# Kernel optimization log

Hardware: AMD Instinct MI355X
Metric: run time of the kernel (lower is better)

## Reference

```python
import jax, jax.numpy as jnp
import numpy as np

WD = 11
HF = WD // 2  # 5

def _offsets():
    # Reproduce the torch module's expanding-ring offset ordering exactly.
    offs = []
    for i in range(1, HF + 1):
        for v in range(HF - i, HF + i + 1):
            for u in range(HF - i, HF + i + 1):
                if not (u == HF and v == HF) and (u, v) not in offs:
                    offs.append((u, v))
    return offs  # length WD*WD-1 = 120

_OFFS = _offsets()


def setup_inputs() -> dict:
    key = jax.random.key(0)
    x = jax.random.normal(key, (2, 3, 384, 1280), dtype=jnp.float32)
    return {"x": x, "attack": 1}


def reference(x, attack):
    n, c, h, w = x.shape
    xm = jnp.mean(x, axis=1)  # [n,h,w] grayscale
    xp = jnp.pad(xm, ((0, 0), (HF, HF), (HF, HF)), mode="reflect")  # [n,h+2*HF,w+2*HF]
    # All 120 shifted views in ring order; static slices, stacked on channel dim.
    shifted = jnp.stack([xp[:, v:v + h, u:u + w] for (u, v) in _OFFS], axis=1)  # [n,120,h,w]
    center = xm[:, None, :, :]
    if attack:
        return jax.nn.sigmoid((shifted - center) * 100000.0)
    return shifted >= center
```

## Files before the change

kernel.cpp:

```cpp
#include <hip/hip_runtime.h>
#include <cstddef>
#include <cstdint>

constexpr int N_  = 2;
constexpr int C_  = 3;
constexpr int H_  = 384;
constexpr int W_  = 1280;
constexpr int HWp = H_ * W_;
constexpr int NOFF = 120;
constexpr int HF_  = 5;

__host__ __device__ constexpr int k_of(int u, int v) {
    int du = u - HF_, dv = v - HF_;
    int au = du < 0 ? -du : du;
    int av = dv < 0 ? -dv : dv;
    int r = au > av ? au : av;
    if (r == 0) return -1;
    int base = (2 * r - 1) * (2 * r - 1) - 1;
    int dv2 = v - (HF_ - r);
    int du2 = u - (HF_ - r);
    int idx = 0;
    if (dv2 == 0)            idx = du2;
    else if (dv2 == 2 * r)   idx = (2 * r + 1) + 2 * (2 * r - 1) + du2;
    else                     idx = (2 * r + 1) + 2 * (dv2 - 1) + (du2 == 0 ? 0 : 1);
    return base + idx;
}

__global__ __launch_bounds__(256) void mean_kernel(const float* __restrict__ x,
                                                   float* __restrict__ xm) {
    int i = blockIdx.x * 256 + threadIdx.x;
    constexpr int TOT4 = N_ * HWp / 4;
    if (i >= TOT4) return;
    int n = i / (HWp / 4);
    int j = i - n * (HWp / 4);
    const float4* x0 = (const float4*)(x + (size_t)n * C_ * HWp);
    const float4* x1 = (const float4*)(x + (size_t)n * C_ * HWp + HWp);
    const float4* x2 = (const float4*)(x + (size_t)n * C_ * HWp + 2 * HWp);
    float4 a = x0[j], b = x1[j], c = x2[j];
    float4 m;
    m.x = (a.x + b.x + c.x) / 3.0f;
    m.y = (a.y + b.y + c.y) / 3.0f;
    m.z = (a.z + b.z + c.z) / 3.0f;
    m.w = (a.w + b.w + c.w) / 3.0f;
    ((float4*)xm)[i] = m;
}

__device__ __forceinline__ float census_val(float s, float center) {
    float d = s - center;
    float r;
    if (__builtin_expect(fabsf(d) >= 1.6e-4f, 1)) {
        r = d > 0.0f ? 1.0f : 0.0f;
    } else {
        float e = __expf(d * -100000.0f);
        r = __builtin_amdgcn_rcpf(1.0f + e);
    }
    return r;
}

__global__ __launch_bounds__(256) void census4_kernel(const float* __restrict__ xm,
                                                      float* __restrict__ out) {
    constexpr int TOT = N_ * HWp / 4;
    int g = blockIdx.x * 256 + threadIdx.x;
    if (g >= TOT) return;
    int n   = g / (HWp / 4);
    int rem = g - n * (HWp / 4);
    int y   = rem / (W_ / 4);
    int x0  = (rem - y * (W_ / 4)) * 4;

    const float* xmn = xm + (size_t)n * HWp;
    float4 c4 = *(const float4*)(xmn + (size_t)y * W_ + x0);

    int xr[14];
#pragma unroll
    for (int j = 0; j < 14; ++j) {
        int xx = x0 - HF_ + j;
        xx = xx < 0 ? -xx : xx;
        xx = xx >= W_ ? 2 * (W_ - 1) - xx : xx;
        xr[j] = xx;
    }

    float* outp = out + (size_t)n * NOFF * HWp + (size_t)y * W_ + x0;

#pragma unroll
    for (int v = 0; v < 11; ++v) {
        int yy = y + v - HF_;
        yy = yy < 0 ? -yy : yy;
        yy = yy >= H_ ? 2 * (H_ - 1) - yy : yy;
        const float* row = xmn + (size_t)yy * W_;

        float s[14];
#pragma unroll
        for (int j = 0; j < 14; ++j) s[j] = row[xr[j]];

#pragma unroll
        for (int u = 0; u < 11; ++u) {
            if (u == HF_ && v == HF_) continue;
            const int k = k_of(u, v);
            float4 r;
            r.x = census_val(s[u + 0], c4.x);
            r.y = census_val(s[u + 1], c4.y);
            r.z = census_val(s[u + 2], c4.z);
            r.w = census_val(s[u + 3], c4.w);
            *(float4*)(outp + (size_t)k * HWp) = r;
        }
    }
}

__device__ __forceinline__ float mean3(const float* __restrict__ xn, int off) {
    return (xn[off] + xn[off + HWp] + xn[off + 2 * HWp]) / 3.0f;
}

__global__ __launch_bounds__(256) void census_fused_kernel(const float* __restrict__ x,
                                                           float* __restrict__ out) {
    int bx = blockIdx.x % 5;
    int t  = blockIdx.x / 5;
    int y  = t % H_;
    int n  = t / H_;
    int xp = bx * 256 + threadIdx.x;

    const float* xn = x + (size_t)n * C_ * HWp;
    float center = mean3(xn, y * W_ + xp);

    int xr[11];
#pragma unroll
    for (int u = 0; u < 11; ++u) {
        int xx = xp + u - HF_;
        xx = xx < 0 ? -xx : xx;
        xx = xx >= W_ ? 2 * (W_ - 1) - xx : xx;
        xr[u] = xx;
    }

    float* outp = out + (size_t)n * NOFF * HWp + (size_t)y * W_ + xp;

#pragma unroll
    for (int v = 0; v < 11; ++v) {
        int yy = y + v - HF_;
        yy = yy < 0 ? -yy : yy;
        yy = yy >= H_ ? 2 * (H_ - 1) - yy : yy;
#pragma unroll
        for (int u = 0; u < 11; ++u) {
            if (u == HF_ && v == HF_) continue;
            const int k = k_of(u, v);
            float s = mean3(xn, yy * W_ + xr[u]);
            outp[(size_t)k * HWp] = census_val(s, center);
        }
    }
}

extern "C" void kernel_launch(void* const* d_in, const int* in_sizes, int n_in,
                              void* d_out, int out_size, void* d_ws, size_t ws_size,
                              hipStream_t stream) {
    const float* x = (const float*)d_in[0];
    float* out = (float*)d_out;

    const size_t xm_bytes = (size_t)N_ * HWp * sizeof(float);

    if (ws_size >= xm_bytes) {
        float* xm = (float*)d_ws;
        const int mean_blocks = (N_ * HWp / 4 + 255) / 256;
        mean_kernel<<<mean_blocks, 256, 0, stream>>>(x, xm);
        const int census_blocks = (N_ * HWp / 4 + 255) / 256;
        census4_kernel<<<census_blocks, 256, 0, stream>>>(xm, out);
    } else {
        const int census_blocks = N_ * H_ * (W_ / 256);
        census_fused_kernel<<<census_blocks, 256, 0, stream>>>(x, out);
    }
}
```

Baseline: 470.8 us.

## Fuse channel mean into census kernel via LDS halo tiles with nontemporal stores

Replaces the separate mean kernel and global-memory census kernel with one kernel. Each block computes the grayscale mean for a 4x256 tile plus its reflect-padded halo into shared memory, then reads neighbours from LDS. Output writes use nontemporal stores so the large output streams past the cache. This removes the intermediate workspace round trip and a kernel launch, at the cost of recomputing halo means, since the 14x266 tile redundantly covers a 4-row output tile.

```diff
diff --git a/kernel.cpp b/kernel.cpp
--- a/kernel.cpp
+++ b/kernel.cpp
@@ -9,6 +9,11 @@
 constexpr int HWp = H_ * W_;
 constexpr int NOFF = 120;
 constexpr int HF_  = 5;
+
+constexpr int TW = 256;
+constexpr int TH = 4;
+constexpr int SW = TW + 2 * HF_;
+constexpr int SH = TH + 2 * HF_;
 
 __host__ __device__ constexpr int k_of(int u, int v) {
     int du = u - HF_, dv = v - HF_;
@@ -26,25 +31,6 @@
     return base + idx;
 }
 
-__global__ __launch_bounds__(256) void mean_kernel(const float* __restrict__ x,
-                                                   float* __restrict__ xm) {
-    int i = blockIdx.x * 256 + threadIdx.x;
-    constexpr int TOT4 = N_ * HWp / 4;
-    if (i >= TOT4) return;
-    int n = i / (HWp / 4);
-    int j = i - n * (HWp / 4);
-    const float4* x0 = (const float4*)(x + (size_t)n * C_ * HWp);
-    const float4* x1 = (const float4*)(x + (size_t)n * C_ * HWp + HWp);
-    const float4* x2 = (const float4*)(x + (size_t)n * C_ * HWp + 2 * HWp);
-    float4 a = x0[j], b = x1[j], c = x2[j];
-    float4 m;
-    m.x = (a.x + b.x + c.x) / 3.0f;
-    m.y = (a.y + b.y + c.y) / 3.0f;
-    m.z = (a.z + b.z + c.z) / 3.0f;
-    m.w = (a.w + b.w + c.w) / 3.0f;
-    ((float4*)xm)[i] = m;
-}
-
 __device__ __forceinline__ float census_val(float s, float center) {
     float d = s - center;
     float r;
@@ -57,92 +43,64 @@
     return r;
 }
 
-__global__ __launch_bounds__(256) void census4_kernel(const float* __restrict__ xm,
-                                                      float* __restrict__ out) {
-    constexpr int TOT = N_ * HWp / 4;
-    int g = blockIdx.x * 256 + threadIdx.x;
-    if (g >= TOT) return;
-    int n   = g / (HWp / 4);
-    int rem = g - n * (HWp / 4);
-    int y   = rem / (W_ / 4);
-    int x0  = (rem - y * (W_ / 4)) * 4;
+typedef float f32x4 __attribute__((ext_vector_type(4)));
 
-    const float* xmn = xm + (size_t)n * HWp;
-    float4 c4 = *(const float4*)(xmn + (size_t)y * W_ + x0);
+__global__ __launch_bounds__(256) void census_fused_lds(const float* __restrict__ x,
+                                                        float* __restrict__ out) {
+    __shared__ float sm[SH][SW];
 
-    int xr[14];
-#pragma unroll
-    for (int j = 0; j < 14; ++j) {
-        int xx = x0 - HF_ + j;
-        xx = xx < 0 ? -xx : xx;
-        xx = xx >= W_ ? 2 * (W_ - 1) - xx : xx;
-        xr[j] = xx;
+    int bx = blockIdx.x % (W_ / TW);
+    int t  = blockIdx.x / (W_ / TW);
+    int yt = t % (H_ / TH);
+    int n  = t / (H_ / TH);
+    int x0 = bx * TW, y0 = yt * TH;
+
+    const float* xn = x + (size_t)n * C_ * HWp;
+
+    for (int idx = threadIdx.x; idx < SH * SW; idx += 256) {
+        int r = idx / SW, c = idx - r * SW;
+        int gy = y0 + r - HF_;
+        gy = gy < 0 ? -gy : gy;
+        gy = gy >= H_ ? 2 * (H_ - 1) - gy : gy;
+        int gx = x0 + c - HF_;
+        gx = gx < 0 ? -gx : gx;
+        gx = gx >= W_ ? 2 * (W_ - 1) - gx : gx;
+        int off = gy * W_ + gx;
+        sm[r][c] = (xn[off] + xn[off + HWp] + xn[off + 2 * HWp]) / 3.0f;
     }
+    __syncthreads();
 
-    float* outp = out + (size_t)n * NOFF * HWp + (size_t)y * W_ + x0;
+    int ty = threadIdx.x >> 6;
+    int tx = (threadIdx.x & 63) * 4;
+    int y  = y0 + ty;
+    int xg = x0 + tx;
+
+    float4 c4;
+    c4.x = sm[HF_ + ty][HF_ + tx + 0];
+    c4.y = sm[HF_ + ty][HF_ + tx + 1];
+    c4.z = sm[HF_ + ty][HF_ + tx + 2];
+    c4.w = sm[HF_ + ty][HF_ + tx + 3];
+
+    float* outp = out + (size_t)n * NOFF * HWp + (size_t)y * W_ + xg;
 
 #pragma unroll
     for (int v = 0; v < 11; ++v) {
-        int yy = y + v - HF_;
-        yy = yy < 0 ? -yy : yy;
-        yy = yy >= H_ ? 2 * (H_ - 1) - yy : yy;
-        const float* row = xmn + (size_t)yy * W_;
+        const float* srow = sm[ty + v];
 
         float s[14];
 #pragma unroll
-        for (int j = 0; j < 14; ++j) s[j] = row[xr[j]];
+        for (int j = 0; j < 14; ++j) s[j] = srow[tx + j];
 
 #pragma unroll
         for (int u = 0; u < 11; ++u) {
             if (u == HF_ && v == HF_) continue;
             const int k = k_of(u, v);
-            float4 r;
+            f32x4 r;
             r.x = census_val(s[u + 0], c4.x);
             r.y = census_val(s[u + 1], c4.y);
             r.z = census_val(s[u + 2], c4.z);
             r.w = census_val(s[u + 3], c4.w);
-            *(float4*)(outp + (size_t)k * HWp) = r;
-        }
-    }
-}
-
-__device__ __forceinline__ float mean3(const float* __restrict__ xn, int off) {
-    return (xn[off] + xn[off + HWp] + xn[off + 2 * HWp]) / 3.0f;
-}
-
-__global__ __launch_bounds__(256) void census_fused_kernel(const float* __restrict__ x,
-                                                           float* __restrict__ out) {
-    int bx = blockIdx.x % 5;
-    int t  = blockIdx.x / 5;
-    int y  = t % H_;
-    int n  = t / H_;
-    int xp = bx * 256 + threadIdx.x;
-
-    const float* xn = x + (size_t)n * C_ * HWp;
-    float center = mean3(xn, y * W_ + xp);
-
-    int xr[11];
-#pragma unroll
-    for (int u = 0; u < 11; ++u) {
-        int xx = xp + u - HF_;
-        xx = xx < 0 ? -xx : xx;
-        xx = xx >= W_ ? 2 * (W_ - 1) - xx : xx;
-        xr[u] = xx;
-    }
-
-    float* outp = out + (size_t)n * NOFF * HWp + (size_t)y * W_ + xp;
-
-#pragma unroll
-    for (int v = 0; v < 11; ++v) {
-        int yy = y + v - HF_;
-        yy = yy < 0 ? -yy : yy;
-        yy = yy >= H_ ? 2 * (H_ - 1) - yy : yy;
-#pragma unroll
-        for (int u = 0; u < 11; ++u) {
-            if (u == HF_ && v == HF_) continue;
-            const int k = k_of(u, v);
-            float s = mean3(xn, yy * W_ + xr[u]);
-            outp[(size_t)k * HWp] = census_val(s, center);
+            __builtin_nontemporal_store(r, (f32x4*)(outp + (size_t)k * HWp));
         }
     }
 }
@@ -153,16 +111,6 @@
     const float* x = (const float*)d_in[0];
     float* out = (float*)d_out;
 
-    const size_t xm_bytes = (size_t)N_ * HWp * sizeof(float);
-
-    if (ws_size >= xm_bytes) {
-        float* xm = (float*)d_ws;
-        const int mean_blocks = (N_ * HWp / 4 + 255) / 256;
-        mean_kernel<<<mean_blocks, 256, 0, stream>>>(x, xm);
-        const int census_blocks = (N_ * HWp / 4 + 255) / 256;
-        census4_kernel<<<census_blocks, 256, 0, stream>>>(xm, out);
-    } else {
-        const int census_blocks = N_ * H_ * (W_ / 256);
-        census_fused_kernel<<<census_blocks, 256, 0, stream>>>(x, out);
-    }
+    const int blocks = N_ * (H_ / TH) * (W_ / TW);
+    census_fused_lds<<<blocks, 256, 0, stream>>>(x, out);
 }
```

Result: no change. 476.8 us (+1.3%).
